# Kernel tuning notes

Measured on AMD Instinct MI355X. Metric: run time of the kernel, lower is better.

The kernel has to match this reference:

```python
import jax, jax.numpy as jnp
import numpy as np

N = 50000        # nodes
E = 640000       # edges
HID = 128        # hidden_channels
HEADS = 2
C = HID // 2     # out_channels per head (64)
ATT_SLOPE = 0.2  # GATv2Conv leaky_relu slope
OUT_SLOPE = 0.01 # F.leaky_relu default slope in GAT.forward


def setup_inputs() -> dict:
    key = jax.random.key(0)
    ks = jax.random.split(key, 11)
    s = 0.05
    return {
        "x": jax.random.normal(ks[0], (N, HID), dtype=jnp.float32),
        "edge_index": jax.random.randint(ks[1], (2, E), 0, N, dtype=jnp.int32),
        # layer 1 params (torch Linear layout: [out, in])
        "w_l1": jax.random.normal(ks[2], (HEADS * C, HID), dtype=jnp.float32) * s,
        "w_r1": jax.random.normal(ks[3], (HEADS * C, HID), dtype=jnp.float32) * s,
        "att1": jax.random.normal(ks[4], (HEADS, C), dtype=jnp.float32) * s,
        "b1": jnp.zeros((HEADS * C,), dtype=jnp.float32),
        # layer 2 params
        "w_l2": jax.random.normal(ks[5], (HEADS * C, HID), dtype=jnp.float32) * s,
        "w_r2": jax.random.normal(ks[6], (HEADS * C, HID), dtype=jnp.float32) * s,
        "att2": jax.random.normal(ks[7], (HEADS, C), dtype=jnp.float32) * s,
        "b2": jnp.zeros((HEADS * C,), dtype=jnp.float32),
    }


def gatv2_conv(x, src, dst, w_l, w_r, att, b):
    # x: [N, HID] -> out: [N, HEADS*C]  (concat=True), dropout inactive (eval)
    x_l = (x @ w_l.T).reshape(N, HEADS, C)  # source transform
    x_r = (x @ w_r.T).reshape(N, HEADS, C)  # target transform
    x_j = x_l[src]                           # [E, H, C] gathered source feats
    e = jax.nn.leaky_relu(x_j + x_r[dst], ATT_SLOPE)
    alpha = jnp.einsum('ehc,hc->eh', e, att)  # [E, H]
    # segment softmax over incoming edges of each target node
    amax = jax.ops.segment_max(alpha, dst, num_segments=N)
    amax = jnp.where(jnp.isfinite(amax), amax, 0.0)
    ex = jnp.exp(alpha - amax[dst])
    denom = jax.ops.segment_sum(ex, dst, num_segments=N)
    alpha = ex / (denom[dst] + 1e-16)
    out = jax.ops.segment_sum(alpha[:, :, None] * x_j, dst, num_segments=N)
    return out.reshape(N, HEADS * C) + b


def reference(x, edge_index, w_l1, w_r1, att1, b1, w_l2, w_r2, att2, b2):
    src, dst = edge_index[0], edge_index[1]
    h1 = jax.nn.leaky_relu(gatv2_conv(x, src, dst, w_l1, w_r1, att1, b1), OUT_SLOPE)
    h2 = gatv2_conv(h1, src, dst, w_l2, w_r2, att2, b2)
    return h1 + h2
```

## Files before the change

kernel.cpp:

```cpp
#include <hip/hip_runtime.h>
#include <hip/hip_bf16.h>
#include <cmath>

#define HID 128
#define ATT_SLOPE 0.2f
#define OUT_SLOPE 0.01f
#define LOG2E 1.44269504f
#define GM 64
#define ASTRIDE 144
#define CSRCAP 64
#define CNTSTRIDE 16

typedef __attribute__((ext_vector_type(8))) short bf16x8;
typedef __attribute__((ext_vector_type(4))) float f32x4;

__device__ __forceinline__ short f2bf(float f) {
    __hip_bfloat16 h = __float2bfloat16(f);
    return *reinterpret_cast<short*>(&h);
}
__device__ __forceinline__ unsigned packbf(float a, float b) {
    return (unsigned)(unsigned short)f2bf(a) | ((unsigned)(unsigned short)f2bf(b) << 16);
}
__device__ __forceinline__ float bflo(unsigned u) { return __uint_as_float(u << 16); }
__device__ __forceinline__ float bfhi(unsigned u) { return __uint_as_float(u & 0xffff0000u); }

__device__ __forceinline__ float fast_exp2(float x) {
#if __has_builtin(__builtin_amdgcn_exp2f)
    return __builtin_amdgcn_exp2f(x);
#else
    return exp2f(x);
#endif
}

__device__ __forceinline__ void gemm_tile(const float* __restrict__ X,
                                          const float* __restrict__ wl,
                                          const float* __restrict__ wr,
                                          unsigned* __restrict__ xlp,
                                          unsigned* __restrict__ xrp,
                                          int nNodes, int tile,
                                          short (*as)[ASTRIDE], int t) {
    int n0 = tile * GM;
    int w = t >> 6, lane = t & 63;
    int q = lane >> 4, ln = lane & 15;

    #pragma unroll
    for (int it = 0; it < 4; ++it) {
        int chunk = it * 256 + t;
        int r = chunk >> 4, c = chunk & 15;
        int gr = n0 + r;
        float4 u4 = make_float4(0.f, 0.f, 0.f, 0.f);
        float4 v4 = make_float4(0.f, 0.f, 0.f, 0.f);
        if (gr < nNodes) {
            const float4* pp = (const float4*)(X + (size_t)gr * HID + c * 8);
            u4 = pp[0]; v4 = pp[1];
        }
        bf16x8 b;
        b[0] = f2bf(u4.x); b[1] = f2bf(u4.y); b[2] = f2bf(u4.z); b[3] = f2bf(u4.w);
        b[4] = f2bf(v4.x); b[5] = f2bf(v4.y); b[6] = f2bf(v4.z); b[7] = f2bf(v4.w);
        *(bf16x8*)&as[r][c * 8] = b;
    }

    bf16x8 bfrag[4][4];
    #pragma unroll
    for (int ct = 0; ct < 4; ++ct) {
        int col = w * 64 + ct * 16 + ln;
        const float* Wp = (col < 128) ? (wl + (size_t)col * HID)
                                      : (wr + (size_t)(col - 128) * HID);
        #pragma unroll
        for (int ks = 0; ks < 4; ++ks) {
            const float4* pp = (const float4*)(Wp + ks * 32 + q * 8);
            float4 u4 = pp[0], v4 = pp[1];
            bf16x8 b;
            b[0] = f2bf(u4.x); b[1] = f2bf(u4.y); b[2] = f2bf(u4.z); b[3] = f2bf(u4.w);
            b[4] = f2bf(v4.x); b[5] = f2bf(v4.y); b[6] = f2bf(v4.z); b[7] = f2bf(v4.w);
            bfrag[ct][ks] = b;
        }
    }
    __syncthreads();

    f32x4 acc[4][4];
    #pragma unroll
    for (int rt = 0; rt < 4; ++rt)
        #pragma unroll
        for (int ct = 0; ct < 4; ++ct) acc[rt][ct] = (f32x4){0.f, 0.f, 0.f, 0.f};

    #pragma unroll
    for (int rt = 0; rt < 4; ++rt) {
        bf16x8 afrag[4];
        #pragma unroll
        for (int ks = 0; ks < 4; ++ks)
            afrag[ks] = *(const bf16x8*)&as[rt * 16 + ln][ks * 32 + q * 8];
        #pragma unroll
        for (int ks = 0; ks < 4; ++ks)
            #pragma unroll
            for (int ct = 0; ct < 4; ++ct)
                acc[rt][ct] = __builtin_amdgcn_mfma_f32_16x16x32_bf16(
                    afrag[ks], bfrag[ct][ks], acc[rt][ct], 0, 0, 0);
    }

    unsigned* dstp = (w < 2) ? xlp : xrp;
    int dbase = (w & 1) * 32 + ln;
    #pragma unroll
    for (int rt = 0; rt < 4; ++rt) {
        #pragma unroll
        for (int c2 = 0; c2 < 2; ++c2) {
            int d = dbase + c2 * 16;
            #pragma unroll
            for (int i = 0; i < 4; ++i) {
                int row = n0 + rt * 16 + q * 4 + i;
                if (row < nNodes)
                    dstp[(size_t)row * 64 + d] = packbf(acc[rt][c2][i], acc[rt][c2 + 2][i]);
            }
        }
    }
}

__global__ __launch_bounds__(256) void fused_g1_fill(const float* __restrict__ X,
                                                     const float* __restrict__ wl,
                                                     const float* __restrict__ wr,
                                                     unsigned* __restrict__ xlp,
                                                     unsigned* __restrict__ xrp,
                                                     const int* __restrict__ src,
                                                     const int* __restrict__ dst,
                                                     int* __restrict__ cnt,
                                                     int* __restrict__ csr,
                                                     int N, int E, int fillb) {
    __shared__ __align__(16) short as[GM][ASTRIDE];
    int bid = blockIdx.x, t = threadIdx.x;
    if (bid >= fillb) {
        gemm_tile(X, wl, wr, xlp, xrp, N, bid - fillb, as, t);
    } else {
        int base = bid * 1024 + t;
        int dd[4], ss[4];
        bool v[4];
        #pragma unroll
        for (int i = 0; i < 4; ++i) {
            int e = base + i * 256;
            v[i] = e < E;
            int ec = v[i] ? e : 0;
            dd[i] = dst[ec];
            ss[i] = src[ec];
        }
        int pp[4];
        #pragma unroll
        for (int i = 0; i < 4; ++i)
            pp[i] = v[i] ? atomicAdd(&cnt[dd[i] << 4], 1) : CSRCAP;
        #pragma unroll
        for (int i = 0; i < 4; ++i)
            if (pp[i] < CSRCAP) csr[(size_t)dd[i] * CSRCAP + pp[i]] = ss[i];
    }
}

__global__ __launch_bounds__(256) void k_gemm(const float* __restrict__ X,
                                              const float* __restrict__ wl,
                                              const float* __restrict__ wr,
                                              unsigned* __restrict__ xlp,
                                              unsigned* __restrict__ xrp, int nNodes) {
    __shared__ __align__(16) short as[GM][ASTRIDE];
    gemm_tile(X, wl, wr, xlp, xrp, nNodes, blockIdx.x, as, threadIdx.x);
}

template <int LAYER>
__global__ __launch_bounds__(256) void gat_edge(const uint4* __restrict__ xlp4,
                                                const uint4* __restrict__ xrp4,
                                                const int* __restrict__ cnt,
                                                const int* __restrict__ csr,
                                                const float* __restrict__ att,
                                                const float* __restrict__ bias,
                                                const float* __restrict__ h1,
                                                float* __restrict__ outp, int nNodes) {
    int n = (int)((blockIdx.x * blockDim.x + threadIdx.x) >> 6);
    int lane = threadIdx.x & 63;
    if (n >= nNodes) return;
    const int slot = lane >> 4;
    const int u = lane & 15;
    const int lo_base = 4 * u + ((u < 8) ? 0 : 32);
    const int* crow = csr + (size_t)n * CSRCAP;

    int dg = cnt[n << 4];
    int sreg = (lane < 32) ? crow[lane] : 0;
    uint4 xrv = xrp4[(size_t)n * 16 + u];

    dg = min(dg, CSRCAP);
    if (lane >= 32 && lane < dg) sreg = crow[lane];

    float a[8], asl[8];
    #pragma unroll
    for (int i = 0; i < 4; ++i) {
        a[2 * i]     = att[lo_base + i] * LOG2E;
        a[2 * i + 1] = att[lo_base + i + 32] * LOG2E;
        asl[2 * i]     = a[2 * i] * ATT_SLOPE;
        asl[2 * i + 1] = a[2 * i + 1] * ATT_SLOPE;
    }

    float xr8[8];
    {
        unsigned xv[4] = {xrv.x, xrv.y, xrv.z, xrv.w};
        #pragma unroll
        for (int i = 0; i < 4; ++i) { xr8[2 * i] = bflo(xv[i]); xr8[2 * i + 1] = bfhi(xv[i]); }
    }

    float l = 0.f, acc[8];
    #pragma unroll
    for (int i = 0; i < 8; ++i) acc[i] = 0.f;

    if (dg > 0) {
        int dgm1 = dg - 1;
        int rounds = (dg + 3) >> 2;
        int s0 = __shfl(sreg, min(slot, dgm1), 64);
        uint4 v0 = xlp4[(size_t)s0 * 16 + u];
        int s1 = __shfl(sreg, min(4 + slot, dgm1), 64);
        uint4 v1 = xlp4[(size_t)s1 * 16 + u];
        for (int g = 0; g < rounds; ++g) {
            uint4 vc = v0;
            v0 = v1;
            int sn = __shfl(sreg, min((g + 2) * 4 + slot, dgm1), 64);
            v1 = xlp4[(size_t)sn * 16 + u];

            bool act = g * 4 + slot < dg;
            unsigned xv[4] = {vc.x, vc.y, vc.z, vc.w};
            float x8[8];
            float pl = 0.f;
            #pragma unroll
            for (int i = 0; i < 4; ++i) {
                float xa = bflo(xv[i]), xb = bfhi(xv[i]);
                x8[2 * i] = xa; x8[2 * i + 1] = xb;
                float ta = xa + xr8[2 * i];
                float tb = xb + xr8[2 * i + 1];
                pl = fmaf(a[2 * i],       fmaxf(ta, 0.f), pl);
                pl = fmaf(asl[2 * i],     fminf(ta, 0.f), pl);
                pl = fmaf(a[2 * i + 1],   fmaxf(tb, 0.f), pl);
                pl = fmaf(asl[2 * i + 1], fminf(tb, 0.f), pl);
            }
            pl += __shfl_xor(pl, 1, 64);
            pl += __shfl_xor(pl, 2, 64);
            pl += __shfl_xor(pl, 4, 64);
            float wgt = act ? fast_exp2(pl) : 0.f;
            l += wgt;
            #pragma unroll
            for (int i = 0; i < 8; ++i) acc[i] = fmaf(wgt, x8[i], acc[i]);
        }
    }

    l += __shfl_xor(l, 32, 64);
    #pragma unroll
    for (int i = 0; i < 8; ++i) acc[i] += __shfl_xor(acc[i], 32, 64);
    l += __shfl_xor(l, 16, 64);
    #pragma unroll
    for (int i = 0; i < 8; ++i) acc[i] += __shfl_xor(acc[i], 16, 64);

    if (lane < 16) {
        size_t nb = (size_t)n * HID;
        float inv = 1.f / (l + 1e-16f);
        const float4 blo = *(const float4*)&bias[lo_base];
        const float4 bhi = *(const float4*)&bias[lo_base + 32];
        float o[8];
        o[0] = acc[0] * inv + blo.x; o[2] = acc[2] * inv + blo.y;
        o[4] = acc[4] * inv + blo.z; o[6] = acc[6] * inv + blo.w;
        o[1] = acc[1] * inv + bhi.x; o[3] = acc[3] * inv + bhi.y;
        o[5] = acc[5] * inv + bhi.z; o[7] = acc[7] * inv + bhi.w;
        if (LAYER == 1) {
            #pragma unroll
            for (int i = 0; i < 8; ++i) o[i] = o[i] > 0.f ? o[i] : OUT_SLOPE * o[i];
        } else {
            const float4 hlo = *(const float4*)&h1[nb + lo_base];
            const float4 hhi = *(const float4*)&h1[nb + lo_base + 32];
            o[0] += hlo.x; o[2] += hlo.y; o[4] += hlo.z; o[6] += hlo.w;
            o[1] += hhi.x; o[3] += hhi.y; o[5] += hhi.z; o[7] += hhi.w;
        }
        *(float4*)&outp[nb + lo_base]      = make_float4(o[0], o[2], o[4], o[6]);
        *(float4*)&outp[nb + lo_base + 32] = make_float4(o[1], o[3], o[5], o[7]);
    }
}

extern "C" void kernel_launch(void* const* d_in, const int* in_sizes, int n_in,
                              void* d_out, int out_size, void* d_ws, size_t ws_size,
                              hipStream_t stream) {
    const float* x    = (const float*)d_in[0];
    const int* ei     = (const int*)d_in[1];
    const float* w_l1 = (const float*)d_in[2];
    const float* w_r1 = (const float*)d_in[3];
    const float* att1 = (const float*)d_in[4];
    const float* b1   = (const float*)d_in[5];
    const float* w_l2 = (const float*)d_in[6];
    const float* w_r2 = (const float*)d_in[7];
    const float* att2 = (const float*)d_in[8];
    const float* b2   = (const float*)d_in[9];

    const int N = in_sizes[0] / HID;
    const int E = in_sizes[1] / 2;
    const int* srcp = ei;
    const int* dstp = ei + E;

    unsigned* xlp = (unsigned*)d_ws;
    unsigned* xrp = xlp + (size_t)N * 64;
    float* h1buf  = (float*)(xrp + (size_t)N * 64);
    int* cnt      = (int*)(h1buf + (size_t)N * HID);
    int* csr      = cnt + (size_t)N * CNTSTRIDE;
    float* outf   = (float*)d_out;

    const int gtiles = (N + GM - 1) / GM;
    const int fillb  = (E + 1023) / 1024;
    const int nblk   = gtiles + fillb;
    const int ab     = (N + 3) / 4;

    hipMemsetAsync(cnt, 0, (size_t)N * CNTSTRIDE * sizeof(int), stream);
    fused_g1_fill<<<nblk, 256, 0, stream>>>(x, w_l1, w_r1, xlp, xrp,
                                            srcp, dstp, cnt, csr, N, E, fillb);
    gat_edge<1><<<ab, 256, 0, stream>>>((const uint4*)xlp, (const uint4*)xrp,
                                        cnt, csr, att1, b1, nullptr, h1buf, N);
    k_gemm<<<gtiles, 256, 0, stream>>>(h1buf, w_l2, w_r2, xlp, xrp, N);
    gat_edge<2><<<ab, 256, 0, stream>>>((const uint4*)xlp, (const uint4*)xrp,
                                        cnt, csr, att2, b2, h1buf, outf, N);
}
```

Measured before the change: 237.7 us.

## Merge all phases into one persistent cooperative kernel with grid syncs

```diff
diff --git a/kernel.cpp b/kernel.cpp
--- a/kernel.cpp
+++ b/kernel.cpp
@@ -1,6 +1,9 @@
 #include <hip/hip_runtime.h>
 #include <hip/hip_bf16.h>
+#include <hip/hip_cooperative_groups.h>
 #include <cmath>
+
+namespace cg = cooperative_groups;
 
 #define HID 128
 #define ATT_SLOPE 0.2f
@@ -115,74 +118,19 @@
     }
 }
 
-__global__ __launch_bounds__(256) void fused_g1_fill(const float* __restrict__ X,
-                                                     const float* __restrict__ wl,
-                                                     const float* __restrict__ wr,
-                                                     unsigned* __restrict__ xlp,
-                                                     unsigned* __restrict__ xrp,
-                                                     const int* __restrict__ src,
-                                                     const int* __restrict__ dst,
-                                                     int* __restrict__ cnt,
-                                                     int* __restrict__ csr,
-                                                     int N, int E, int fillb) {
-    __shared__ __align__(16) short as[GM][ASTRIDE];
-    int bid = blockIdx.x, t = threadIdx.x;
-    if (bid >= fillb) {
-        gemm_tile(X, wl, wr, xlp, xrp, N, bid - fillb, as, t);
-    } else {
-        int base = bid * 1024 + t;
-        int dd[4], ss[4];
-        bool v[4];
-        #pragma unroll
-        for (int i = 0; i < 4; ++i) {
-            int e = base + i * 256;
-            v[i] = e < E;
-            int ec = v[i] ? e : 0;
-            dd[i] = dst[ec];
-            ss[i] = src[ec];
-        }
-        int pp[4];
-        #pragma unroll
-        for (int i = 0; i < 4; ++i)
-            pp[i] = v[i] ? atomicAdd(&cnt[dd[i] << 4], 1) : CSRCAP;
-        #pragma unroll
-        for (int i = 0; i < 4; ++i)
-            if (pp[i] < CSRCAP) csr[(size_t)dd[i] * CSRCAP + pp[i]] = ss[i];
-    }
-}
-
-__global__ __launch_bounds__(256) void k_gemm(const float* __restrict__ X,
-                                              const float* __restrict__ wl,
-                                              const float* __restrict__ wr,
-                                              unsigned* __restrict__ xlp,
-                                              unsigned* __restrict__ xrp, int nNodes) {
-    __shared__ __align__(16) short as[GM][ASTRIDE];
-    gemm_tile(X, wl, wr, xlp, xrp, nNodes, blockIdx.x, as, threadIdx.x);
-}
-
 template <int LAYER>
-__global__ __launch_bounds__(256) void gat_edge(const uint4* __restrict__ xlp4,
-                                                const uint4* __restrict__ xrp4,
-                                                const int* __restrict__ cnt,
-                                                const int* __restrict__ csr,
-                                                const float* __restrict__ att,
-                                                const float* __restrict__ bias,
-                                                const float* __restrict__ h1,
-                                                float* __restrict__ outp, int nNodes) {
-    int n = (int)((blockIdx.x * blockDim.x + threadIdx.x) >> 6);
-    int lane = threadIdx.x & 63;
-    if (n >= nNodes) return;
+__device__ __forceinline__ void gat_phase(const uint4* __restrict__ xlp4,
+                                          const uint4* __restrict__ xrp4,
+                                          const int* __restrict__ cnt,
+                                          const int* __restrict__ csr,
+                                          const float* __restrict__ att,
+                                          const float* __restrict__ bias,
+                                          const float* __restrict__ h1,
+                                          float* __restrict__ outp,
+                                          int nNodes, int wv, int nwaves, int lane) {
     const int slot = lane >> 4;
     const int u = lane & 15;
     const int lo_base = 4 * u + ((u < 8) ? 0 : 32);
-    const int* crow = csr + (size_t)n * CSRCAP;
-
-    int dg = cnt[n << 4];
-    int sreg = (lane < 32) ? crow[lane] : 0;
-    uint4 xrv = xrp4[(size_t)n * 16 + u];
-
-    dg = min(dg, CSRCAP);
-    if (lane >= 32 && lane < dg) sreg = crow[lane];
 
     float a[8], asl[8];
     #pragma unroll
@@ -192,85 +140,162 @@
         asl[2 * i]     = a[2 * i] * ATT_SLOPE;
         asl[2 * i + 1] = a[2 * i + 1] * ATT_SLOPE;
     }
-
-    float xr8[8];
-    {
-        unsigned xv[4] = {xrv.x, xrv.y, xrv.z, xrv.w};
-        #pragma unroll
-        for (int i = 0; i < 4; ++i) { xr8[2 * i] = bflo(xv[i]); xr8[2 * i + 1] = bfhi(xv[i]); }
-    }
-
-    float l = 0.f, acc[8];
-    #pragma unroll
-    for (int i = 0; i < 8; ++i) acc[i] = 0.f;
-
-    if (dg > 0) {
-        int dgm1 = dg - 1;
-        int rounds = (dg + 3) >> 2;
-        int s0 = __shfl(sreg, min(slot, dgm1), 64);
-        uint4 v0 = xlp4[(size_t)s0 * 16 + u];
-        int s1 = __shfl(sreg, min(4 + slot, dgm1), 64);
-        uint4 v1 = xlp4[(size_t)s1 * 16 + u];
-        for (int g = 0; g < rounds; ++g) {
-            uint4 vc = v0;
-            v0 = v1;
-            int sn = __shfl(sreg, min((g + 2) * 4 + slot, dgm1), 64);
-            v1 = xlp4[(size_t)sn * 16 + u];
-
-            bool act = g * 4 + slot < dg;
-            unsigned xv[4] = {vc.x, vc.y, vc.z, vc.w};
-            float x8[8];
-            float pl = 0.f;
+    const float4 blo = *(const float4*)&bias[lo_base];
+    const float4 bhi = *(const float4*)&bias[lo_base + 32];
+
+    for (int n = wv; n < nNodes; n += nwaves) {
+        const int* crow = csr + (size_t)n * CSRCAP;
+        int dg = cnt[n << 4];
+        int sreg = (lane < 32) ? crow[lane] : 0;
+        uint4 xrv = xrp4[(size_t)n * 16 + u];
+        dg = min(dg, CSRCAP);
+        if (lane >= 32 && lane < dg) sreg = crow[lane];
+
+        float xr8[8];
+        {
+            unsigned xv[4] = {xrv.x, xrv.y, xrv.z, xrv.w};
             #pragma unroll
-            for (int i = 0; i < 4; ++i) {
-                float xa = bflo(xv[i]), xb = bfhi(xv[i]);
-                x8[2 * i] = xa; x8[2 * i + 1] = xb;
-                float ta = xa + xr8[2 * i];
-                float tb = xb + xr8[2 * i + 1];
-                pl = fmaf(a[2 * i],       fmaxf(ta, 0.f), pl);
-                pl = fmaf(asl[2 * i],     fminf(ta, 0.f), pl);
-                pl = fmaf(a[2 * i + 1],   fmaxf(tb, 0.f), pl);
-                pl = fmaf(asl[2 * i + 1], fminf(tb, 0.f), pl);
+            for (int i = 0; i < 4; ++i) { xr8[2 * i] = bflo(xv[i]); xr8[2 * i + 1] = bfhi(xv[i]); }
+        }
+
+        float l = 0.f, acc[8];
+        #pragma unroll
+        for (int i = 0; i < 8; ++i) acc[i] = 0.f;
+
+        if (dg > 0) {
+            int dgm1 = dg - 1;
+            int rounds = (dg + 3) >> 2;
+            int s0 = __shfl(sreg, min(slot, dgm1), 64);
+            uint4 v0 = xlp4[(size_t)s0 * 16 + u];
+            int s1 = __shfl(sreg, min(4 + slot, dgm1), 64);
+            uint4 v1 = xlp4[(size_t)s1 * 16 + u];
+            for (int g = 0; g < rounds; ++g) {
+                uint4 vc = v0;
+                v0 = v1;
+                int sn = __shfl(sreg, min((g + 2) * 4 + slot, dgm1), 64);
+                v1 = xlp4[(size_t)sn * 16 + u];
+
+                bool act = g * 4 + slot < dg;
+                unsigned xv[4] = {vc.x, vc.y, vc.z, vc.w};
+                float x8[8];
+                float pl = 0.f;
+                #pragma unroll
+                for (int i = 0; i < 4; ++i) {
+                    float xa = bflo(xv[i]), xb = bfhi(xv[i]);
+                    x8[2 * i] = xa; x8[2 * i + 1] = xb;
+                    float ta = xa + xr8[2 * i];
+                    float tb = xb + xr8[2 * i + 1];
+                    pl = fmaf(a[2 * i],       fmaxf(ta, 0.f), pl);
+                    pl = fmaf(asl[2 * i],     fminf(ta, 0.f), pl);
+                    pl = fmaf(a[2 * i + 1],   fmaxf(tb, 0.f), pl);
+                    pl = fmaf(asl[2 * i + 1], fminf(tb, 0.f), pl);
+                }
+                pl += __shfl_xor(pl, 1, 64);
+                pl += __shfl_xor(pl, 2, 64);
+                pl += __shfl_xor(pl, 4, 64);
+                float wgt = act ? fast_exp2(pl) : 0.f;
+                l += wgt;
+                #pragma unroll
+                for (int i = 0; i < 8; ++i) acc[i] = fmaf(wgt, x8[i], acc[i]);
             }
-            pl += __shfl_xor(pl, 1, 64);
-            pl += __shfl_xor(pl, 2, 64);
-            pl += __shfl_xor(pl, 4, 64);
-            float wgt = act ? fast_exp2(pl) : 0.f;
-            l += wgt;
-            #pragma unroll
-            for (int i = 0; i < 8; ++i) acc[i] = fmaf(wgt, x8[i], acc[i]);
-        }
-    }
-
-    l += __shfl_xor(l, 32, 64);
-    #pragma unroll
-    for (int i = 0; i < 8; ++i) acc[i] += __shfl_xor(acc[i], 32, 64);
-    l += __shfl_xor(l, 16, 64);
-    #pragma unroll
-    for (int i = 0; i < 8; ++i) acc[i] += __shfl_xor(acc[i], 16, 64);
-
-    if (lane < 16) {
-        size_t nb = (size_t)n * HID;
-        float inv = 1.f / (l + 1e-16f);
-        const float4 blo = *(const float4*)&bias[lo_base];
-        const float4 bhi = *(const float4*)&bias[lo_base + 32];
-        float o[8];
-        o[0] = acc[0] * inv + blo.x; o[2] = acc[2] * inv + blo.y;
-        o[4] = acc[4] * inv + blo.z; o[6] = acc[6] * inv + blo.w;
-        o[1] = acc[1] * inv + bhi.x; o[3] = acc[3] * inv + bhi.y;
-        o[5] = acc[5] * inv + bhi.z; o[7] = acc[7] * inv + bhi.w;
-        if (LAYER == 1) {
-            #pragma unroll
-            for (int i = 0; i < 8; ++i) o[i] = o[i] > 0.f ? o[i] : OUT_SLOPE * o[i];
-        } else {
-            const float4 hlo = *(const float4*)&h1[nb + lo_base];
-            const float4 hhi = *(const float4*)&h1[nb + lo_base + 32];
-            o[0] += hlo.x; o[2] += hlo.y; o[4] += hlo.z; o[6] += hlo.w;
-            o[1] += hhi.x; o[3] += hhi.y; o[5] += hhi.z; o[7] += hhi.w;
-        }
-        *(float4*)&outp[nb + lo_base]      = make_float4(o[0], o[2], o[4], o[6]);
-        *(float4*)&outp[nb + lo_base + 32] = make_float4(o[1], o[3], o[5], o[7]);
-    }
+        }
+
+        l += __shfl_xor(l, 32, 64);
+        #pragma unroll
+        for (int i = 0; i < 8; ++i) acc[i] += __shfl_xor(acc[i], 32, 64);
+        l += __shfl_xor(l, 16, 64);
+        #pragma unroll
+        for (int i = 0; i < 8; ++i) acc[i] += __shfl_xor(acc[i], 16, 64);
+
+        if (lane < 16) {
+            size_t nb2 = (size_t)n * HID;
+            float inv = 1.f / (l + 1e-16f);
+            float o[8];
+            o[0] = acc[0] * inv + blo.x; o[2] = acc[2] * inv + blo.y;
+            o[4] = acc[4] * inv + blo.z; o[6] = acc[6] * inv + blo.w;
+            o[1] = acc[1] * inv + bhi.x; o[3] = acc[3] * inv + bhi.y;
+            o[5] = acc[5] * inv + bhi.z; o[7] = acc[7] * inv + bhi.w;
+            if (LAYER == 1) {
+                #pragma unroll
+                for (int i = 0; i < 8; ++i) o[i] = o[i] > 0.f ? o[i] : OUT_SLOPE * o[i];
+            } else {
+                const float4 hlo = *(const float4*)&h1[nb2 + lo_base];
+                const float4 hhi = *(const float4*)&h1[nb2 + lo_base + 32];
+                o[0] += hlo.x; o[2] += hlo.y; o[4] += hlo.z; o[6] += hlo.w;
+                o[1] += hhi.x; o[3] += hhi.y; o[5] += hhi.z; o[7] += hhi.w;
+            }
+            *(float4*)&outp[nb2 + lo_base]      = make_float4(o[0], o[2], o[4], o[6]);
+            *(float4*)&outp[nb2 + lo_base + 32] = make_float4(o[1], o[3], o[5], o[7]);
+        }
+    }
+}
+
+__global__ __launch_bounds__(256, 4) void gat_all(
+        const float* __restrict__ X,
+        const int* __restrict__ src, const int* __restrict__ dst,
+        const float* __restrict__ wl1, const float* __restrict__ wr1,
+        const float* __restrict__ att1, const float* __restrict__ b1,
+        const float* __restrict__ wl2, const float* __restrict__ wr2,
+        const float* __restrict__ att2, const float* __restrict__ b2,
+        unsigned* __restrict__ xlp, unsigned* __restrict__ xrp,
+        float* __restrict__ h1, int* __restrict__ cnt, int* __restrict__ csr,
+        float* __restrict__ outp, int N, int E, int gtiles) {
+    __shared__ __align__(16) short as[GM][ASTRIDE];
+    cg::grid_group grid = cg::this_grid();
+    const int bid = blockIdx.x, t = threadIdx.x, nb = gridDim.x;
+    const int tid = bid * 256 + t, tot = nb * 256;
+    const int lane = t & 63;
+    const int wv = tid >> 6, nwaves = tot >> 6;
+
+    for (int i = tid; i < N * CNTSTRIDE / 4; i += tot)
+        ((int4*)cnt)[i] = make_int4(0, 0, 0, 0);
+    __threadfence();
+    grid.sync();
+
+    int dd[4], ss[4], pp[4];
+    bool vv[4];
+    #pragma unroll
+    for (int i = 0; i < 4; ++i) {
+        int e = tid + i * tot;
+        vv[i] = e < E;
+        int ec = vv[i] ? e : 0;
+        dd[i] = dst[ec];
+        ss[i] = src[ec];
+    }
+    #pragma unroll
+    for (int i = 0; i < 4; ++i)
+        pp[i] = vv[i] ? atomicAdd(&cnt[dd[i] << 4], 1) : CSRCAP;
+
+    for (int tile = bid; tile < gtiles; tile += nb) {
+        gemm_tile(X, wl1, wr1, xlp, xrp, N, tile, as, t);
+        __syncthreads();
+    }
+
+    #pragma unroll
+    for (int i = 0; i < 4; ++i)
+        if (pp[i] < CSRCAP) csr[(size_t)dd[i] * CSRCAP + pp[i]] = ss[i];
+    for (int e = tid + 4 * tot; e < E; e += tot) {
+        int d2 = dst[e], s2 = src[e];
+        int p2 = atomicAdd(&cnt[d2 << 4], 1);
+        if (p2 < CSRCAP) csr[(size_t)d2 * CSRCAP + p2] = s2;
+    }
+    __threadfence();
+    grid.sync();
+
+    gat_phase<1>((const uint4*)xlp, (const uint4*)xrp, cnt, csr, att1, b1,
+                 nullptr, h1, N, wv, nwaves, lane);
+    __threadfence();
+    grid.sync();
+
+    for (int tile = bid; tile < gtiles; tile += nb) {
+        gemm_tile(h1, wl2, wr2, xlp, xrp, N, tile, as, t);
+        __syncthreads();
+    }
+    __threadfence();
+    grid.sync();
+
+    gat_phase<2>((const uint4*)xlp, (const uint4*)xrp, cnt, csr, att2, b2,
+                 h1, outp, N, wv, nwaves, lane);
 }
 
 extern "C" void kernel_launch(void* const* d_in, const int* in_sizes, int n_in,
@@ -299,17 +324,27 @@
     int* csr      = cnt + (size_t)N * CNTSTRIDE;
     float* outf   = (float*)d_out;
 
-    const int gtiles = (N + GM - 1) / GM;
-    const int fillb  = (E + 1023) / 1024;
-    const int nblk   = gtiles + fillb;
-    const int ab     = (N + 3) / 4;
-
-    hipMemsetAsync(cnt, 0, (size_t)N * CNTSTRIDE * sizeof(int), stream);
-    fused_g1_fill<<<nblk, 256, 0, stream>>>(x, w_l1, w_r1, xlp, xrp,
-                                            srcp, dstp, cnt, csr, N, E, fillb);
-    gat_edge<1><<<ab, 256, 0, stream>>>((const uint4*)xlp, (const uint4*)xrp,
-                                        cnt, csr, att1, b1, nullptr, h1buf, N);
-    k_gemm<<<gtiles, 256, 0, stream>>>(h1buf, w_l2, w_r2, xlp, xrp, N);
-    gat_edge<2><<<ab, 256, 0, stream>>>((const uint4*)xlp, (const uint4*)xrp,
-                                        cnt, csr, att2, b2, h1buf, outf, N);
-}
+    int gtiles = (N + GM - 1) / GM;
+
+    static int gridBlocks = 0;
+    if (gridBlocks == 0) {
+        hipDeviceProp_t prop;
+        hipGetDeviceProperties(&prop, 0);
+        int perCu = 0;
+        hipOccupancyMaxActiveBlocksPerMultiprocessor(&perCu, gat_all, 256, 0);
+        if (perCu < 1) perCu = 1;
+        long g = (long)perCu * prop.multiProcessorCount;
+        gridBlocks = (int)(g < 1024 ? g : 1024);
+    }
+
+    int Nv = N, Ev = E, gt = gtiles;
+    void* args[] = {
+        (void*)&x, (void*)&srcp, (void*)&dstp,
+        (void*)&w_l1, (void*)&w_r1, (void*)&att1, (void*)&b1,
+        (void*)&w_l2, (void*)&w_r2, (void*)&att2, (void*)&b2,
+        (void*)&xlp, (void*)&xrp, (void*)&h1buf, (void*)&cnt, (void*)&csr,
+        (void*)&outf, (void*)&Nv, (void*)&Ev, (void*)&gt,
+    };
+    hipLaunchCooperativeKernel((const void*)gat_all, dim3(gridBlocks), dim3(256),
+                               args, 0, stream);
+}
```

Result: slower. 832.9 us (+250.4%).
